# Performance work log

Measured on AMD Instinct MI355X. Metric: run time of the kernel, lower is better.

## Reference

```python
import jax, jax.numpy as jnp
import numpy as np

EMBED = 1024
HEADS = 16
HEAD_DIM = EMBED // HEADS


def setup_inputs() -> dict:
    key = jax.random.key(0)
    kx, kq, kk, kv, ko = jax.random.split(key, 5)
    s = 1.0 / np.sqrt(EMBED)
    return {
        "x": jax.random.normal(kx, (4, 2048, EMBED), dtype=jnp.float32),
        "Wq": jax.random.uniform(kq, (EMBED, EMBED), jnp.float32, -s, s),
        "Wk": jax.random.uniform(kk, (EMBED, EMBED), jnp.float32, -s, s),
        "Wv": jax.random.uniform(kv, (EMBED, EMBED), jnp.float32, -s, s),
        "Wo": jax.random.uniform(ko, (EMBED, EMBED), jnp.float32, -s, s),
    }


def reference(x, Wq, Wk, Wv, Wo):
    B, S, E = x.shape
    # nn.Linear computes x @ W.T; weights stored as (out, in)
    q = (x @ Wq.T).reshape(B, S, HEADS, HEAD_DIM).transpose(0, 2, 1, 3)  # [B,H,S,D]
    k = (x @ Wk.T).reshape(B, S, HEADS, HEAD_DIM).transpose(0, 2, 1, 3)
    v = (x @ Wv.T).reshape(B, S, HEADS, HEAD_DIM).transpose(0, 2, 1, 3)
    scores = jnp.einsum("bhsd,bhtd->bhst", q, k) / np.sqrt(HEAD_DIM)  # [B,H,S,S]
    causal = jnp.triu(jnp.ones((S, S), dtype=bool), k=1)
    scores = jnp.where(causal[None, None], -jnp.inf, scores)
    probs = jax.nn.softmax(scores, axis=-1)  # dropout_rate=0 -> identity
    attn = jnp.einsum("bhst,bhtd->bhsd", probs, v)  # [B,H,S,D]
    attn = attn.transpose(0, 2, 1, 3).reshape(B, S, E)
    return attn @ Wo.T
```

## Files before the change

kernel.cpp:

```cpp
#include <hip/hip_runtime.h>

#define EMB 1024
#define NHEADS 16
#define HD 64
#define BATCH 4
#define SEQ 2048
#define MTOK (BATCH*SEQ)

typedef __bf16 bf16x8 __attribute__((ext_vector_type(8)));
typedef __bf16 bf16x4 __attribute__((ext_vector_type(4)));
typedef float  f32x4  __attribute__((ext_vector_type(4)));

#define MFMA16(a,b,c) __builtin_amdgcn_mfma_f32_16x16x32_bf16(a,b,c,0,0,0)

__device__ __forceinline__ void gload_lds16(const __bf16* g, __bf16* l) {
    __builtin_amdgcn_global_load_lds(
        (__attribute__((address_space(1))) void*)(g),
        (__attribute__((address_space(3))) void*)(l), 16, 0, 0);
}

__global__ void cvt_all(const float* __restrict__ x,  const float* __restrict__ wq,
                        const float* __restrict__ wk, const float* __restrict__ wv,
                        const float* __restrict__ wo,
                        __bf16* xb, __bf16* wqb, __bf16* wkb, __bf16* wvb, __bf16* wob) {
    int z = blockIdx.y;
    const float* src = (z == 0) ? x : (z == 1) ? wq : (z == 2) ? wk : (z == 3) ? wv : wo;
    __bf16*      dst = (z == 0) ? xb : (z == 1) ? wqb : (z == 2) ? wkb : (z == 3) ? wvb : wob;
    int n = (z == 0) ? MTOK * EMB : EMB * EMB;
    int i = (blockIdx.x * blockDim.x + threadIdx.x) * 4;
    if (i < n) {
        float4 v = *(const float4*)(src + i);
        bf16x4 o = { (__bf16)v.x, (__bf16)v.y, (__bf16)v.z, (__bf16)v.w };
        *(bf16x4*)(dst + i) = o;
    }
}

__global__ __launch_bounds__(256) void transpose_v(const __bf16* __restrict__ vb,
                                                   __bf16* __restrict__ vt) {
    __shared__ __bf16 t[64 * 72];
    const int tid = threadIdx.x;
    const int bh = blockIdx.y, s0 = blockIdx.x * 64;
    const __bf16* src = vb + ((size_t)bh * SEQ + s0) * HD;
    int sr = tid >> 3, cc = (tid & 7) * 8;
    bf16x8 a0 = *(const bf16x8*)(src + (size_t)sr * HD + cc);
    bf16x8 a1 = *(const bf16x8*)(src + (size_t)(sr + 32) * HD + cc);
    *(bf16x8*)(t + sr * 72 + cc)        = a0;
    *(bf16x8*)(t + (sr + 32) * 72 + cc) = a1;
    __syncthreads();
    int dr = tid >> 3, g = tid & 7;
    __bf16* dstb = vt + (size_t)bh * HD * SEQ + s0;
    #pragma unroll
    for (int it = 0; it < 2; ++it) {
        int d = dr + it * 32;
        bf16x8 o;
        #pragma unroll
        for (int j = 0; j < 8; ++j) o[j] = t[(g * 8 + j) * 72 + d];
        *(bf16x8*)(dstb + (size_t)d * SEQ + g * 8) = o;
    }
}

__device__ __forceinline__ void gemm_bt_body(
    const __bf16* __restrict__ A, const __bf16* __restrict__ Bw,
    int tileM, int tileN, __bf16* As, __bf16* Bs, f32x4 acc[4][4])
{
    const int tid   = threadIdx.x;
    const int w     = tid >> 6;
    const int lane  = tid & 63;
    const int mlane = lane & 15;
    const int quad  = lane >> 4;
    const int wm    = (w >> 1) * 64;
    const int wn    = (w & 1) * 64;

    const f32x4 fzero = {0.f, 0.f, 0.f, 0.f};
    #pragma unroll
    for (int mi = 0; mi < 4; ++mi)
        #pragma unroll
        for (int ni = 0; ni < 4; ++ni) acc[mi][ni] = fzero;

    for (int kt = 0; kt < EMB; kt += 32) {
        #pragma unroll
        for (int i = 0; i < 2; ++i) {
            int cbase = i * 256 + w * 64;
            int c  = cbase + lane;
            int m  = c >> 2;
            int dq = (c & 3) ^ ((m >> 1) & 3);
            gload_lds16(A  + (size_t)(tileM + m) * EMB + kt + dq * 8, As + cbase * 8);
            gload_lds16(Bw + (size_t)(tileN + m) * EMB + kt + dq * 8, Bs + cbase * 8);
        }
        asm volatile("s_waitcnt vmcnt(0)" ::: "memory");
        __syncthreads();

        bf16x8 af[4], bfr[4];
        #pragma unroll
        for (int mi = 0; mi < 4; ++mi) {
            int row = wm + mi * 16 + mlane;
            af[mi] = *(const bf16x8*)(As + row * 32 + ((quad ^ ((row >> 1) & 3)) * 8));
        }
        #pragma unroll
        for (int ni = 0; ni < 4; ++ni) {
            int row = wn + ni * 16 + mlane;
            bfr[ni] = *(const bf16x8*)(Bs + row * 32 + ((quad ^ ((row >> 1) & 3)) * 8));
        }
        #pragma unroll
        for (int mi = 0; mi < 4; ++mi)
            #pragma unroll
            for (int ni = 0; ni < 4; ++ni)
                acc[mi][ni] = MFMA16(af[mi], bfr[ni], acc[mi][ni]);
        __syncthreads();
    }
}

__global__ __launch_bounds__(256) void qkv_gemm(
    const __bf16* __restrict__ xb,
    const __bf16* __restrict__ wq, const __bf16* __restrict__ wk, const __bf16* __restrict__ wv,
    __bf16* __restrict__ Qb, __bf16* __restrict__ Kb, __bf16* __restrict__ Vb)
{
    __shared__ __bf16 As[128 * 32];
    __shared__ __bf16 Bs[128 * 32];
    const int z = blockIdx.z;
    const __bf16* W = (z == 0) ? wq : (z == 1) ? wk : wv;
    __bf16* O       = (z == 0) ? Qb : (z == 1) ? Kb : Vb;
    const float scl = (z == 0) ? 0.18033688011112042f : 1.0f;

    f32x4 acc[4][4];
    gemm_bt_body(xb, W, blockIdx.y * 128, blockIdx.x * 128, As, Bs, acc);

    const int tid = threadIdx.x, w = tid >> 6, lane = tid & 63;
    const int mlane = lane & 15, quad = lane >> 4;
    const int wm = (w >> 1) * 64, wn = (w & 1) * 64;
    #pragma unroll
    for (int mi = 0; mi < 4; ++mi) {
        #pragma unroll
        for (int ni = 0; ni < 4; ++ni) {
            int ncol = blockIdx.x * 128 + wn + ni * 16 + mlane;
            int h = ncol >> 6, d = ncol & 63;
            #pragma unroll
            for (int r = 0; r < 4; ++r) {
                int mr = blockIdx.y * 128 + wm + mi * 16 + quad * 4 + r;
                int b = mr >> 11, s = mr & 2047;
                O[(((size_t)b * NHEADS + h) * SEQ + s) * HD + d] = (__bf16)(acc[mi][ni][r] * scl);
            }
        }
    }
}

__global__ __launch_bounds__(256) void out_gemm(
    const __bf16* __restrict__ attnb, const __bf16* __restrict__ wo, float* __restrict__ out)
{
    __shared__ __bf16 As[128 * 32];
    __shared__ __bf16 Bs[128 * 32];
    f32x4 acc[4][4];
    gemm_bt_body(attnb, wo, blockIdx.y * 128, blockIdx.x * 128, As, Bs, acc);

    const int tid = threadIdx.x, w = tid >> 6, lane = tid & 63;
    const int mlane = lane & 15, quad = lane >> 4;
    const int wm = (w >> 1) * 64, wn = (w & 1) * 64;
    #pragma unroll
    for (int mi = 0; mi < 4; ++mi) {
        #pragma unroll
        for (int ni = 0; ni < 4; ++ni) {
            int ncol = blockIdx.x * 128 + wn + ni * 16 + mlane;
            #pragma unroll
            for (int r = 0; r < 4; ++r) {
                int mr = blockIdx.y * 128 + wm + mi * 16 + quad * 4 + r;
                out[(size_t)mr * EMB + ncol] = acc[mi][ni][r];
            }
        }
    }
}

__global__ __launch_bounds__(512, 1) void attn_kernel(
    const __bf16* __restrict__ Qb, const __bf16* __restrict__ Kb,
    const __bf16* __restrict__ Vtg, __bf16* __restrict__ attnb)
{
    __shared__ __bf16 Ks[2 * 64 * 64];
    __shared__ __bf16 Vs[2 * 64 * 64];
    __shared__ __bf16 Ps[8 * 16 * 72];

    const int tid = threadIdx.x, w = tid >> 6, lane = tid & 63;
    const int mlane = lane & 15, quad = lane >> 4;
    const int h = blockIdx.y, b = blockIdx.z;
    const size_t headoff = ((size_t)b * NHEADS + h) * SEQ * HD;
    const __bf16* Qg = Qb + headoff;
    const __bf16* Kg = Kb + headoff;
    const __bf16* Vg = Vtg + headoff;
    __bf16* Psw = Ps + w * 16 * 72;
    const int g0 = quad ^ (mlane & 7);
    const f32x4 fzero = {0.f, 0.f, 0.f, 0.f};

    const int st_row = tid >> 3;
    const int st_cc  = (tid & 7) ^ (st_row & 7);
    const int st_dst = (tid & ~63) * 8;

    for (int sp = 0; sp < 2; ++sp) {
        const int strip = sp ? (15 - (int)blockIdx.x) : (int)blockIdx.x;
        const int qw  = strip * 128 + w * 16;
        const int nch = 2 * strip + 2;

        __syncthreads();

        gload_lds16(Kg + (size_t)st_row * HD + st_cc * 8, Ks + st_dst);
        gload_lds16(Vg + (size_t)st_row * SEQ + st_cc * 8, Vs + st_dst);

        bf16x8 bq0 = *(const bf16x8*)(Qg + (size_t)(qw + mlane) * HD + quad * 8);
        bf16x8 bq1 = *(const bf16x8*)(Qg + (size_t)(qw + mlane) * HD + 32 + quad * 8);

        float l_acc = 0.f;
        f32x4 o[4];
        #pragma unroll
        for (int dt = 0; dt < 4; ++dt) o[dt] = fzero;

        for (int c = 0; c < nch; ++c) {
            const int tb = c * 64;
            const __bf16* Kp = Ks + (c & 1) * 4096;
            const __bf16* Vp = Vs + (c & 1) * 4096;
            __bf16* Kn = Ks + ((c & 1) ^ 1) * 4096;
            __bf16* Vn = Vs + ((c & 1) ^ 1) * 4096;

            asm volatile("s_waitcnt vmcnt(0)" ::: "memory");
            __syncthreads();

            if (c + 1 < nch) {
                const int tbn = tb + 64;
                gload_lds16(Kg + (size_t)(tbn + st_row) * HD + st_cc * 8, Kn + st_dst);
                gload_lds16(Vg + (size_t)st_row * SEQ + tbn + st_cc * 8, Vn + st_dst);
            }

            const int rel = qw + 15 - tb;
            if (rel >= 0) {
                f32x4 s[4];
                #pragma unroll
                for (int mt = 0; mt < 4; ++mt) {
                    const __bf16* ka = Kp + (mt * 16 + mlane) * 64;
                    bf16x8 ak0 = *(const bf16x8*)(ka + g0 * 8);
                    bf16x8 ak1 = *(const bf16x8*)(ka + (g0 ^ 4) * 8);
                    s[mt] = MFMA16(ak1, bq1, MFMA16(ak0, bq0, fzero));
                }
                if (rel < 78) {
                    const int qrel = qw + mlane - tb - quad * 4;
                    #pragma unroll
                    for (int mt = 0; mt < 4; ++mt)
                        #pragma unroll
                        for (int r = 0; r < 4; ++r)
                            if (mt * 16 + r > qrel) s[mt][r] = -3e38f;
                }

                f32x4 vsum = fzero;
                #pragma unroll
                for (int mt = 0; mt < 4; ++mt) {
                    #pragma unroll
                    for (int r = 0; r < 4; ++r)
                        s[mt][r] = __builtin_amdgcn_exp2f(s[mt][r]);
                    vsum += s[mt];
                    bf16x4 pb = { (__bf16)s[mt][0], (__bf16)s[mt][1],
                                  (__bf16)s[mt][2], (__bf16)s[mt][3] };
                    *(bf16x4*)(Psw + mlane * 72 + mt * 16 + quad * 4) = pb;
                }
                l_acc += (vsum[0] + vsum[1]) + (vsum[2] + vsum[3]);

                #pragma unroll
                for (int ks = 0; ks < 2; ++ks) {
                    bf16x8 ap = *(const bf16x8*)(Psw + mlane * 72 + ks * 32 + quad * 8);
                    #pragma unroll
                    for (int dt = 0; dt < 4; ++dt) {
                        const __bf16* va = Vp + (dt * 16 + mlane) * 64;
                        bf16x8 bv = *(const bf16x8*)(va + (((ks * 4 + quad) ^ (mlane & 7)) * 8));
                        o[dt] = MFMA16(ap, bv, o[dt]);
                    }
                }
            }
        }

        float lf = l_acc;
        lf += __shfl_xor(lf, 16);
        lf += __shfl_xor(lf, 32);
        #pragma unroll
        for (int r = 0; r < 4; ++r) {
            float lr = __shfl(lf, quad * 4 + r);
            float linv = 1.0f / lr;
            int q = qw + quad * 4 + r;
            size_t rowoff = ((size_t)b * SEQ + q) * EMB + h * HD;
            #pragma unroll
            for (int dt = 0; dt < 4; ++dt)
                attnb[rowoff + dt * 16 + mlane] = (__bf16)(o[dt][r] * linv);
        }
    }
}

extern "C" void kernel_launch(void* const* d_in, const int* in_sizes, int n_in,
                              void* d_out, int out_size, void* d_ws, size_t ws_size,
                              hipStream_t stream) {
    const float* x  = (const float*)d_in[0];
    const float* Wq = (const float*)d_in[1];
    const float* Wk = (const float*)d_in[2];
    const float* Wv = (const float*)d_in[3];
    const float* Wo = (const float*)d_in[4];
    float* out = (float*)d_out;

    char* ws = (char*)d_ws;
    __bf16* xb    = (__bf16*)(ws);
    __bf16* wqb   = (__bf16*)(ws + 16777216);
    __bf16* wkb   = (__bf16*)(ws + 18874368);
    __bf16* wvb   = (__bf16*)(ws + 20971520);
    __bf16* wob   = (__bf16*)(ws + 23068672);
    __bf16* qb    = (__bf16*)(ws + 25165824);
    __bf16* kb    = (__bf16*)(ws + 41943040);
    __bf16* vb    = (__bf16*)(ws + 58720256);
    __bf16* attnb = (__bf16*)(ws + 75497472);
    __bf16* vtb   = xb;

    cvt_all<<<dim3(8192, 5), 256, 0, stream>>>(x, Wq, Wk, Wv, Wo, xb, wqb, wkb, wvb, wob);

    qkv_gemm<<<dim3(EMB / 128, MTOK / 128, 3), 256, 0, stream>>>(xb, wqb, wkb, wvb, qb, kb, vb);

    transpose_v<<<dim3(SEQ / 64, BATCH * NHEADS), 256, 0, stream>>>(vb, vtb);

    attn_kernel<<<dim3(8, NHEADS, BATCH), 512, 0, stream>>>(qb, kb, vtb, attnb);

    out_gemm<<<dim3(EMB / 128, MTOK / 128, 1), 256, 0, stream>>>(attnb, wob, out);
}
```

Before: 258.8 us.

## Rewrite projection GEMMs as 8-phase pipelined 256-tile kernels with fused QKV weights

Replaces the simple 128x128, single-buffered, BK=32 GEMM with a 512-thread, 256xBN-tile GEMM. It double-buffers BK=64 slices in LDS and interleaves async global-to-LDS loads with MFMA phases, using sched barriers and setprio. The QKV projection now treats Wq/Wk/Wv as one contiguous 3072-row weight, relying on their adjacent workspace placement, and remaps blocks for L2 locality. The goal is to hide load latency and raise data reuse per tile, at the cost of more LDS and registers, and a fixed assumption about the weight layout.

```diff
diff --git a/kernel.cpp b/kernel.cpp
--- a/kernel.cpp
+++ b/kernel.cpp
@@ -59,112 +59,217 @@
     }
 }
 
-__device__ __forceinline__ void gemm_bt_body(
-    const __bf16* __restrict__ A, const __bf16* __restrict__ Bw,
-    int tileM, int tileN, __bf16* As, __bf16* Bs, f32x4 acc[4][4])
+
+#define SCHEDB() __builtin_amdgcn_sched_barrier(0)
+#define PH_MID()                                                        \
+    do { SCHEDB(); __builtin_amdgcn_s_barrier();                        \
+         asm volatile("s_waitcnt lgkmcnt(0)" ::: "memory");             \
+         SCHEDB(); __builtin_amdgcn_s_setprio(1); } while (0)
+#define PH_END()                                                        \
+    do { __builtin_amdgcn_s_setprio(0); SCHEDB();                       \
+         __builtin_amdgcn_s_barrier(); SCHEDB(); } while (0)
+#define PH_END_VM0()                                                    \
+    do { __builtin_amdgcn_s_setprio(0); SCHEDB();                       \
+         asm volatile("s_waitcnt vmcnt(0)" ::: "memory");               \
+         __builtin_amdgcn_s_barrier(); SCHEDB(); } while (0)
+#define PH_END_VM2()                                                    \
+    do { __builtin_amdgcn_s_setprio(0); SCHEDB();                       \
+         asm volatile("s_waitcnt vmcnt(2)" ::: "memory");               \
+         __builtin_amdgcn_s_barrier(); SCHEDB(); } while (0)
+
+#define MMAQ(AF, BF, MH, NHI)                                           \
+    do {                                                                \
+        _Pragma("unroll")                                               \
+        for (int m_ = 0; m_ < 4; ++m_) {                                \
+            _Pragma("unroll")                                           \
+            for (int n_ = 0; n_ < NH; ++n_) {                           \
+                f32x4 c_ = acc[(MH)*4 + m_][(NHI)*NH + n_];             \
+                c_ = MFMA16(AF[m_][0], BF[n_][0], c_);                  \
+                c_ = MFMA16(AF[m_][1], BF[n_][1], c_);                  \
+                acc[(MH)*4 + m_][(NHI)*NH + n_] = c_;                   \
+            }                                                           \
+        }                                                               \
+    } while (0)
+
+template<int BN>
+__device__ __forceinline__ void gemm8ph(
+    const __bf16* __restrict__ Ag,
+    const __bf16* __restrict__ Bg,
+    __bf16* __restrict__ As, __bf16* __restrict__ Bs,
+    f32x4 (&acc)[8][BN/64])
 {
+    constexpr int NH    = BN / 128;
+    constexpr int BSLOT = BN * 64;
+
     const int tid   = threadIdx.x;
     const int w     = tid >> 6;
-    const int lane  = tid & 63;
-    const int mlane = lane & 15;
-    const int quad  = lane >> 4;
-    const int wm    = (w >> 1) * 64;
-    const int wn    = (w & 1) * 64;
-
-    const f32x4 fzero = {0.f, 0.f, 0.f, 0.f};
+    const int mlane = tid & 15;
+    const int quad  = (tid >> 4) & 3;
+    const int wm    = w >> 2;
+    const int wn    = w & 3;
+
+    const int rho = mlane & 7;
+    const int e0  = (quad ^ rho) * 8;
+    const int aA0 = mlane * 64 + e0;
+    const int aB0 = (wn * (BN / 4) + mlane) * 64 + e0;
+
+    const int so = (tid >> 3) * 1024 + (((tid & 7) ^ ((tid >> 3) & 7)) * 8);
+    const int sd = (tid & ~63) * 8;
+
+    const auto stA = [&](int slot, int half, int kt) {
+        const __bf16* g = Ag + half * 131072 + kt + so;
+        __bf16* l = As + slot * 16384 + half * 8192 + sd;
+        gload_lds16(g, l);
+        gload_lds16(g + 65536, l + 4096);
+    };
+    const auto stB = [&](int slot, int half, int kt) {
+        const __bf16* g = Bg + half * 131072 + kt + so;
+        __bf16* l = Bs + slot * BSLOT + half * 8192 + sd;
+        gload_lds16(g, l);
+        gload_lds16(g + 65536, l + 4096);
+    };
+    const auto rdA = [&](bf16x8 (&dst)[4][2], int slot, int grp) {
+        const __bf16* base = As + slot * 16384 + wm * 8192 + grp * 4096;
+        #pragma unroll
+        for (int m = 0; m < 4; ++m) {
+            dst[m][0] = *(const bf16x8*)(base + m * 1024 + aA0);
+            dst[m][1] = *(const bf16x8*)(base + m * 1024 + (aA0 ^ 32));
+        }
+    };
+    const auto rdB = [&](bf16x8 (&dst)[NH][2], int slot, int nh) {
+        const __bf16* base = Bs + slot * BSLOT + nh * (NH * 1024);
+        #pragma unroll
+        for (int n = 0; n < NH; ++n) {
+            dst[n][0] = *(const bf16x8*)(base + n * 1024 + aB0);
+            dst[n][1] = *(const bf16x8*)(base + n * 1024 + (aB0 ^ 32));
+        }
+    };
+
+    const f32x4 fz = {0.f, 0.f, 0.f, 0.f};
     #pragma unroll
-    for (int mi = 0; mi < 4; ++mi)
-        #pragma unroll
-        for (int ni = 0; ni < 4; ++ni) acc[mi][ni] = fzero;
-
-    for (int kt = 0; kt < EMB; kt += 32) {
-        #pragma unroll
-        for (int i = 0; i < 2; ++i) {
-            int cbase = i * 256 + w * 64;
-            int c  = cbase + lane;
-            int m  = c >> 2;
-            int dq = (c & 3) ^ ((m >> 1) & 3);
-            gload_lds16(A  + (size_t)(tileM + m) * EMB + kt + dq * 8, As + cbase * 8);
-            gload_lds16(Bw + (size_t)(tileN + m) * EMB + kt + dq * 8, Bs + cbase * 8);
-        }
-        asm volatile("s_waitcnt vmcnt(0)" ::: "memory");
-        __syncthreads();
-
-        bf16x8 af[4], bfr[4];
-        #pragma unroll
-        for (int mi = 0; mi < 4; ++mi) {
-            int row = wm + mi * 16 + mlane;
-            af[mi] = *(const bf16x8*)(As + row * 32 + ((quad ^ ((row >> 1) & 3)) * 8));
-        }
-        #pragma unroll
-        for (int ni = 0; ni < 4; ++ni) {
-            int row = wn + ni * 16 + mlane;
-            bfr[ni] = *(const bf16x8*)(Bs + row * 32 + ((quad ^ ((row >> 1) & 3)) * 8));
-        }
-        #pragma unroll
-        for (int mi = 0; mi < 4; ++mi)
-            #pragma unroll
-            for (int ni = 0; ni < 4; ++ni)
-                acc[mi][ni] = MFMA16(af[mi], bfr[ni], acc[mi][ni]);
-        __syncthreads();
-    }
-}
-
-__global__ __launch_bounds__(256) void qkv_gemm(
-    const __bf16* __restrict__ xb,
-    const __bf16* __restrict__ wq, const __bf16* __restrict__ wk, const __bf16* __restrict__ wv,
+    for (int i = 0; i < 8; ++i)
+        #pragma unroll
+        for (int j = 0; j < BN / 64; ++j) acc[i][j] = fz;
+
+    bf16x8 afA[4][2], afB[4][2], bfA[NH][2], bfB[NH][2];
+
+    stA(0, 0, 0); stA(0, 1, 0); stB(0, 0, 0);
+    if (BN == 256) stB(0, 1, 0);
+    stA(1, 0, 64);
+    asm volatile("s_waitcnt vmcnt(2)" ::: "memory");
+    SCHEDB(); __builtin_amdgcn_s_barrier(); SCHEDB();
+
+    #pragma unroll 1
+    for (int t = 0; t < 8; ++t) {
+        const bool last = (t == 7);
+        const int ktc1 = t * 128 + 64;
+        const int ktn0 = t * 128 + 128;
+        const int ktn1 = t * 128 + 192;
+
+        rdA(afA, 0, 0); rdB(bfA, 0, 0);
+        stA(1, 1, ktc1);
+        PH_MID(); MMAQ(afA, bfA, 0, 0); PH_END();
+
+        rdB(bfB, 0, 1);
+        stB(1, 0, ktc1);
+        PH_MID(); MMAQ(afA, bfB, 0, 1); PH_END();
+
+        rdA(afB, 0, 1);
+        if (BN == 256) stB(1, 1, ktc1);
+        PH_MID(); MMAQ(afB, bfB, 1, 1); PH_END();
+
+        if (!last) stA(0, 0, ktn0);
+        PH_MID(); MMAQ(afB, bfA, 1, 0);
+        if (last) PH_END_VM0(); else PH_END_VM2();
+
+        rdA(afA, 1, 0); rdB(bfA, 1, 0);
+        if (!last) stA(0, 1, ktn0);
+        PH_MID(); MMAQ(afA, bfA, 0, 0); PH_END();
+
+        rdB(bfB, 1, 1);
+        if (!last) stB(0, 0, ktn0);
+        PH_MID(); MMAQ(afA, bfB, 0, 1); PH_END();
+
+        rdA(afB, 1, 1);
+        if (!last && BN == 256) stB(0, 1, ktn0);
+        PH_MID(); MMAQ(afB, bfB, 1, 1); PH_END();
+
+        if (!last) stA(1, 0, ktn1);
+        PH_MID(); MMAQ(afB, bfA, 1, 0);
+        if (last) PH_END(); else PH_END_VM2();
+    }
+}
+
+__global__ __launch_bounds__(512, 2) void qkv_gemm(
+    const __bf16* __restrict__ xb, const __bf16* __restrict__ wqkv,
     __bf16* __restrict__ Qb, __bf16* __restrict__ Kb, __bf16* __restrict__ Vb)
 {
-    __shared__ __bf16 As[128 * 32];
-    __shared__ __bf16 Bs[128 * 32];
-    const int z = blockIdx.z;
-    const __bf16* W = (z == 0) ? wq : (z == 1) ? wk : wv;
-    __bf16* O       = (z == 0) ? Qb : (z == 1) ? Kb : Vb;
-    const float scl = (z == 0) ? 0.18033688011112042f : 1.0f;
-
-    f32x4 acc[4][4];
-    gemm_bt_body(xb, W, blockIdx.y * 128, blockIdx.x * 128, As, Bs, acc);
-
-    const int tid = threadIdx.x, w = tid >> 6, lane = tid & 63;
-    const int mlane = lane & 15, quad = lane >> 4;
-    const int wm = (w >> 1) * 64, wn = (w & 1) * 64;
+    __shared__ __bf16 As[2 * 256 * 64];
+    __shared__ __bf16 Bs[2 * 256 * 64];
+
+    const int bid   = blockIdx.x;
+    const int local = bid >> 3;
+    const int mt    = (bid & 7) * 4 + (local & 3);
+    const int nt    = local >> 2;
+
+    f32x4 acc[8][4];
+    gemm8ph<256>(xb + (size_t)mt * 262144, wqkv + (size_t)nt * 262144, As, Bs, acc);
+
+    const int tid = threadIdx.x, w = tid >> 6;
+    const int mlane = tid & 15, quad = (tid >> 4) & 3;
+    const int wm = w >> 2, wn = w & 3;
+    const int rowb = mt * 256 + wm * 128;
+    const int colb = nt * 256 + wn * 64;
+
     #pragma unroll
-    for (int mi = 0; mi < 4; ++mi) {
-        #pragma unroll
-        for (int ni = 0; ni < 4; ++ni) {
-            int ncol = blockIdx.x * 128 + wn + ni * 16 + mlane;
-            int h = ncol >> 6, d = ncol & 63;
+    for (int ni = 0; ni < 4; ++ni) {
+        int gcol = colb + (ni >> 1) * 32 + (ni & 1) * 16 + mlane;
+        int z = gcol >> 10, cc = gcol & 1023;
+        int h = cc >> 6, d = cc & 63;
+        __bf16* O = (z == 0) ? Qb : (z == 1) ? Kb : Vb;
+        float scl = (z == 0) ? 0.18033688011112042f : 1.0f;
+        #pragma unroll
+        for (int mi = 0; mi < 8; ++mi) {
+            int grow = rowb + (mi >> 2) * 64 + (mi & 3) * 16 + quad * 4;
+            int b = grow >> 11, s = grow & 2047;
             #pragma unroll
-            for (int r = 0; r < 4; ++r) {
-                int mr = blockIdx.y * 128 + wm + mi * 16 + quad * 4 + r;
-                int b = mr >> 11, s = mr & 2047;
-                O[(((size_t)b * NHEADS + h) * SEQ + s) * HD + d] = (__bf16)(acc[mi][ni][r] * scl);
-            }
-        }
-    }
-}
-
-__global__ __launch_bounds__(256) void out_gemm(
-    const __bf16* __restrict__ attnb, const __bf16* __restrict__ wo, float* __restrict__ out)
+            for (int r = 0; r < 4; ++r)
+                O[(((size_t)b * NHEADS + h) * SEQ + (s + r)) * HD + d] =
+                    (__bf16)(acc[mi][ni][r] * scl);
+        }
+    }
+}
+
+__global__ __launch_bounds__(512, 2) void out_gemm(
+    const __bf16* __restrict__ attnb, const __bf16* __restrict__ wo,
+    float* __restrict__ out)
 {
-    __shared__ __bf16 As[128 * 32];
-    __shared__ __bf16 Bs[128 * 32];
-    f32x4 acc[4][4];
-    gemm_bt_body(attnb, wo, blockIdx.y * 128, blockIdx.x * 128, As, Bs, acc);
-
-    const int tid = threadIdx.x, w = tid >> 6, lane = tid & 63;
-    const int mlane = lane & 15, quad = lane >> 4;
-    const int wm = (w >> 1) * 64, wn = (w & 1) * 64;
+    __shared__ __bf16 As[2 * 256 * 64];
+    __shared__ __bf16 Bs[2 * 128 * 64];
+
+    const int bid   = blockIdx.x;
+    const int local = bid >> 3;
+    const int mt    = (bid & 7) * 4 + (local & 3);
+    const int nt    = local >> 2;
+
+    f32x4 acc[8][2];
+    gemm8ph<128>(attnb + (size_t)mt * 262144, wo + (size_t)nt * 131072, As, Bs, acc);
+
+    const int tid = threadIdx.x, w = tid >> 6;
+    const int mlane = tid & 15, quad = (tid >> 4) & 3;
+    const int wm = w >> 2, wn = w & 3;
+    const int rowb = mt * 256 + wm * 128;
+    const int colb = nt * 128 + wn * 32;
+
     #pragma unroll
-    for (int mi = 0; mi < 4; ++mi) {
-        #pragma unroll
-        for (int ni = 0; ni < 4; ++ni) {
-            int ncol = blockIdx.x * 128 + wn + ni * 16 + mlane;
+    for (int mi = 0; mi < 8; ++mi) {
+        int grow = rowb + (mi >> 2) * 64 + (mi & 3) * 16 + quad * 4;
+        #pragma unroll
+        for (int ni = 0; ni < 2; ++ni) {
+            int gcol = colb + ni * 16 + mlane;
             #pragma unroll
-            for (int r = 0; r < 4; ++r) {
-                int mr = blockIdx.y * 128 + wm + mi * 16 + quad * 4 + r;
-                out[(size_t)mr * EMB + ncol] = acc[mi][ni][r];
-            }
+            for (int r = 0; r < 4; ++r)
+                out[(size_t)(grow + r) * EMB + gcol] = acc[mi][ni][r];
         }
     }
 }
@@ -311,11 +416,11 @@
 
     cvt_all<<<dim3(8192, 5), 256, 0, stream>>>(x, Wq, Wk, Wv, Wo, xb, wqb, wkb, wvb, wob);
 
-    qkv_gemm<<<dim3(EMB / 128, MTOK / 128, 3), 256, 0, stream>>>(xb, wqb, wkb, wvb, qb, kb, vb);
+    qkv_gemm<<<dim3(384), 512, 0, stream>>>(xb, wqb, qb, kb, vb);
 
     transpose_v<<<dim3(SEQ / 64, BATCH * NHEADS), 256, 0, stream>>>(vb, vtb);
 
     attn_kernel<<<dim3(8, NHEADS, BATCH), 512, 0, stream>>>(qb, kb, vtb, attnb);
 
-    out_gemm<<<dim3(EMB / 128, MTOK / 128, 1), 256, 0, stream>>>(attnb, wob, out);
-}
+    out_gemm<<<dim3(256), 512, 0, stream>>>(attnb, wob, out);
+}
```

New measurement: 264.9 us. 1.02x slower.
